# Kernel optimization log

Measured on AMD Instinct MI355X. Metric: run time of the kernel, lower is better.

Reference implementation:

```python
import jax, jax.numpy as jnp
import numpy as np

D = 512
N = 2048

def setup_inputs() -> dict:
    key = jax.random.key(0)
    ks = jax.random.split(key, 5)
    scale = 1.0 / np.sqrt(D)
    return {
        "h": jax.random.normal(ks[0], (N, D), dtype=jnp.float32),
        "W_Q": jax.random.normal(ks[1], (D, D), dtype=jnp.float32) * scale,
        "W_K": jax.random.normal(ks[2], (D, D), dtype=jnp.float32) * scale,
        "W_V": jax.random.normal(ks[3], (D, D), dtype=jnp.float32) * scale,
        "W_O": jax.random.normal(ks[4], (D, D), dtype=jnp.float32) * scale,
    }

def reference(h, W_Q, W_K, W_V, W_O):
    d = h.shape[-1]
    inv_sqrt_d = 1.0 / jnp.sqrt(jnp.asarray(d, h.dtype))
    # nn.Linear(d,d,bias=False): y = h @ W.T
    q = h @ W_Q.T  # [N, d]
    k = h @ W_K.T  # [N, d]
    v = h @ W_V.T  # [N, d]
    # per-token outer product q_a * k_b, softmax over b
    scores = (q[:, :, None] * k[:, None, :]) * inv_sqrt_d  # [N, d, d]
    M = jax.nn.softmax(scores, axis=-1)
    o = jnp.einsum("nab,nb->na", M, v)  # [N, d]
    return o @ W_O.T
```

## Files before the change

### kernel.cpp

```cpp
#include <hip/hip_runtime.h>
#include <hip/hip_bf16.h>

typedef __bf16 bf16_t;
typedef __bf16 bf16x8 __attribute__((ext_vector_type(8)));
typedef __bf16 bf16x4 __attribute__((ext_vector_type(4)));
typedef float  f32x4  __attribute__((ext_vector_type(4)));

#define DD    512
#define NTOK  2048
#define P_DEG 12
#define STR   40

__global__ __launch_bounds__(256) void cvt_kernel(
    const float* __restrict__ h, const float* __restrict__ Wq,
    const float* __restrict__ Wk, const float* __restrict__ Wv,
    const float* __restrict__ Wo, bf16_t* __restrict__ hb, bf16_t* __restrict__ Wb)
{
    int idx = blockIdx.x * 256 + threadIdx.x;
    const float* src;
    bf16_t* dst;
    int off;
    if (idx < 262144) { src = h; dst = hb; off = idx; }
    else {
        int r = idx - 262144;
        int w = r >> 16;
        off = r & 65535;
        src = (w == 0) ? Wq : (w == 1) ? Wk : (w == 2) ? Wv : Wo;
        dst = Wb + (size_t)w * DD * DD;
    }
    f32x4 v = reinterpret_cast<const f32x4*>(src)[off];
    bf16x4 o;
    o[0] = (bf16_t)v[0]; o[1] = (bf16_t)v[1]; o[2] = (bf16_t)v[2]; o[3] = (bf16_t)v[3];
    reinterpret_cast<bf16x4*>(dst)[off] = o;
}

__global__ __launch_bounds__(256) void qkv_kernel(
    const bf16_t* __restrict__ hb, const bf16_t* __restrict__ Wb,
    float* __restrict__ Q, float* __restrict__ Kp, float* __restrict__ V)
{
    __shared__ bf16_t sA[128 * STR];
    __shared__ bf16_t sB[64 * STR];

    const int tid  = threadIdx.x;
    const int lane = tid & 63;
    const int wvi  = tid >> 6;
    const int fr   = lane & 15;
    const int q4   = lane >> 4;
    const int kg   = q4 * 8;
    const int mBase = blockIdx.x * 128;
    const int nBase = blockIdx.y * 64;
    const int z    = blockIdx.z;
    const bf16_t* Bm = Wb + (size_t)z * DD * DD + (size_t)nBase * DD;
    float* C = (z == 0) ? Q : (z == 1) ? Kp : V;
    const float scale = (z == 1) ? 0.04419417382415922f : 1.0f;

    f32x4 acc[2][4] = {};

    for (int k0 = 0; k0 < DD; k0 += 32) {
        __syncthreads();
        #pragma unroll
        for (int i = 0; i < 2; i++) {
            int c = tid + i * 256, row = c >> 2, kc = (c & 3) * 8;
            *reinterpret_cast<uint4*>(&sA[row * STR + kc]) =
                *reinterpret_cast<const uint4*>(hb + (size_t)(mBase + row) * DD + k0 + kc);
        }
        {
            int row = tid >> 2, kc = (tid & 3) * 8;
            *reinterpret_cast<uint4*>(&sB[row * STR + kc]) =
                *reinterpret_cast<const uint4*>(Bm + (size_t)row * DD + k0 + kc);
        }
        __syncthreads();

        bf16x8 af[2], bfr[4];
        #pragma unroll
        for (int t = 0; t < 2; t++)
            af[t] = *reinterpret_cast<const bf16x8*>(&sA[(wvi * 32 + t * 16 + fr) * STR + kg]);
        #pragma unroll
        for (int t = 0; t < 4; t++)
            bfr[t] = *reinterpret_cast<const bf16x8*>(&sB[(t * 16 + fr) * STR + kg]);
        #pragma unroll
        for (int ti = 0; ti < 2; ti++)
            #pragma unroll
            for (int tj = 0; tj < 4; tj++)
                acc[ti][tj] = __builtin_amdgcn_mfma_f32_16x16x32_bf16(af[ti], bfr[tj], acc[ti][tj], 0, 0, 0);
    }

    #pragma unroll
    for (int ti = 0; ti < 2; ti++)
        #pragma unroll
        for (int tj = 0; tj < 4; tj++)
            #pragma unroll
            for (int r = 0; r < 4; r++) {
                int gm = mBase + wvi * 32 + ti * 16 + q4 * 4 + r;
                int gn = nBase + tj * 16 + fr;
                C[(size_t)gm * DD + gn] = acc[ti][tj][r] * scale;
            }
}

__global__ __launch_bounds__(256) void out_kernel(
    const bf16_t* __restrict__ O, const bf16_t* __restrict__ Wob, float* __restrict__ out)
{
    __shared__ bf16_t sA[64 * STR];
    __shared__ bf16_t sB[64 * STR];

    const int tid  = threadIdx.x;
    const int lane = tid & 63;
    const int wvi  = tid >> 6;
    const int fr   = lane & 15;
    const int q4   = lane >> 4;
    const int kg   = q4 * 8;
    const int mBase = blockIdx.x * 64, nBase = blockIdx.y * 64;

    f32x4 acc[4] = {};

    for (int k0 = 0; k0 < DD; k0 += 32) {
        __syncthreads();
        {
            int row = tid >> 2, kc = (tid & 3) * 8;
            *reinterpret_cast<uint4*>(&sA[row * STR + kc]) =
                *reinterpret_cast<const uint4*>(O + (size_t)(mBase + row) * DD + k0 + kc);
            *reinterpret_cast<uint4*>(&sB[row * STR + kc]) =
                *reinterpret_cast<const uint4*>(Wob + (size_t)(nBase + row) * DD + k0 + kc);
        }
        __syncthreads();

        bf16x8 af = *reinterpret_cast<const bf16x8*>(&sA[(wvi * 16 + fr) * STR + kg]);
        #pragma unroll
        for (int tj = 0; tj < 4; tj++) {
            bf16x8 bf = *reinterpret_cast<const bf16x8*>(&sB[(tj * 16 + fr) * STR + kg]);
            acc[tj] = __builtin_amdgcn_mfma_f32_16x16x32_bf16(af, bf, acc[tj], 0, 0, 0);
        }
    }

    #pragma unroll
    for (int tj = 0; tj < 4; tj++)
        #pragma unroll
        for (int r = 0; r < 4; r++) {
            int gm = mBase + wvi * 16 + q4 * 4 + r;
            int gn = nBase + tj * 16 + fr;
            out[(size_t)gm * DD + gn] = acc[tj][r];
        }
}

__global__ __launch_bounds__(256) void attn_kernel(
    const float* __restrict__ Q, const float* __restrict__ Kp,
    const float* __restrict__ V, bf16_t* __restrict__ O)
{
    const int n    = blockIdx.x * 4 + (threadIdx.x >> 6);
    const int lane = threadIdx.x & 63;
    const float* kr = Kp + (size_t)n * DD + lane * 8;
    const float* vr = V  + (size_t)n * DD + lane * 8;

    f32x4 k0 = *reinterpret_cast<const f32x4*>(kr);
    f32x4 k1 = *reinterpret_cast<const f32x4*>(kr + 4);
    f32x4 v0 = *reinterpret_cast<const f32x4*>(vr);
    f32x4 v1 = *reinterpret_cast<const f32x4*>(vr + 4);
    float kap[8] = {k0[0], k0[1], k0[2], k0[3], k1[0], k1[1], k1[2], k1[3]};
    float vv[8]  = {v0[0], v0[1], v0[2], v0[3], v1[0], v1[1], v1[2], v1[3]};

    float md[P_DEG + 1] = {}, mc[P_DEG + 1] = {};
    #pragma unroll
    for (int j = 0; j < 8; j++) {
        float p = 1.f;
        #pragma unroll
        for (int t = 0; t <= P_DEG; t++) {
            md[t] += p;
            mc[t] = fmaf(vv[j], p, mc[t]);
            p *= kap[j];
        }
    }
    #pragma unroll
    for (int m = 32; m >= 1; m >>= 1)
        #pragma unroll
        for (int t = 0; t <= P_DEG; t++) {
            md[t] += __shfl_xor(md[t], m);
            mc[t] += __shfl_xor(mc[t], m);
        }

    const float INVF[P_DEG + 1] = {1.f, 1.f, 0.5f, 1.f/6.f, 1.f/24.f, 1.f/120.f,
        1.f/720.f, 1.f/5040.f, 1.f/40320.f, 1.f/362880.f, 1.f/3628800.f,
        1.f/39916800.f, 1.f/479001600.f};
    #pragma unroll
    for (int t = 0; t <= P_DEG; t++) { md[t] *= INVF[t]; mc[t] *= INVF[t]; }

    const float* qr = Q + (size_t)n * DD + lane * 8;
    f32x4 q0 = *reinterpret_cast<const f32x4*>(qr);
    f32x4 q1 = *reinterpret_cast<const f32x4*>(qr + 4);
    float qv[8] = {q0[0], q0[1], q0[2], q0[3], q1[0], q1[1], q1[2], q1[3]};

    bf16x8 ov;
    #pragma unroll
    for (int j = 0; j < 8; j++) {
        float x = qv[j];
        float F = mc[P_DEG], G = md[P_DEG];
        #pragma unroll
        for (int t = P_DEG - 1; t >= 0; t--) {
            F = fmaf(F, x, mc[t]);
            G = fmaf(G, x, md[t]);
        }
        ov[j] = (bf16_t)(F * __builtin_amdgcn_rcpf(G));
    }
    *reinterpret_cast<bf16x8*>(O + (size_t)n * DD + lane * 8) = ov;
}

extern "C" void kernel_launch(void* const* d_in, const int* in_sizes, int n_in,
                              void* d_out, int out_size, void* d_ws, size_t ws_size,
                              hipStream_t stream)
{
    const float* h  = (const float*)d_in[0];
    const float* Wq = (const float*)d_in[1];
    const float* Wk = (const float*)d_in[2];
    const float* Wv = (const float*)d_in[3];
    const float* Wo = (const float*)d_in[4];
    float* out = (float*)d_out;

    float*  Q  = (float*)d_ws;
    float*  Kp = Q  + (size_t)NTOK * DD;
    float*  V  = Kp + (size_t)NTOK * DD;
    bf16_t* O  = (bf16_t*)(V + (size_t)NTOK * DD);
    bf16_t* hb = O  + (size_t)NTOK * DD;
    bf16_t* Wb = hb + (size_t)NTOK * DD;

    cvt_kernel<<<dim3(2048), dim3(256), 0, stream>>>(h, Wq, Wk, Wv, Wo, hb, Wb);
    qkv_kernel<<<dim3(NTOK / 128, DD / 64, 3), dim3(256), 0, stream>>>(hb, Wb, Q, Kp, V);
    attn_kernel<<<dim3(NTOK / 4), dim3(256), 0, stream>>>(Q, Kp, V, O);
    out_kernel<<<dim3(NTOK / 64, DD / 64), dim3(256), 0, stream>>>(
        O, Wb + (size_t)3 * DD * DD, out);
}
```

Measured before the change: 94.80 us.

## Double-buffer GEMMs with direct global-to-LDS loads and swizzled LDS layout

Both projection GEMMs now stage tiles with global_load_lds into double-buffered, XOR-swizzled shared memory. Each K step of 64 is prefetched while the previous one is consumed, and smaller M tiles give more blocks. The attention kernel hoists the Q load, uses DPP for the first two reduction steps, and skips the constant degree-0 denominator term. The aim is to hide global-load latency, remove bank conflicts and cut shuffle cost, at the price of more LDS per block and a dependence on the global_load_lds lane-address mapping being correct.

```diff
diff --git a/kernel.cpp b/kernel.cpp
--- a/kernel.cpp
+++ b/kernel.cpp
@@ -5,11 +5,24 @@
 typedef __bf16 bf16x8 __attribute__((ext_vector_type(8)));
 typedef __bf16 bf16x4 __attribute__((ext_vector_type(4)));
 typedef float  f32x4  __attribute__((ext_vector_type(4)));
+typedef unsigned int u32;
 
 #define DD    512
 #define NTOK  2048
 #define P_DEG 12
-#define STR   40
+
+__device__ __forceinline__ void gl_lds16(const bf16_t* g, bf16_t* l) {
+    __builtin_amdgcn_global_load_lds((const u32*)g, (u32*)l, 16, 0, 0);
+}
+
+__device__ __forceinline__ float dpp_add_x1(float x) {
+    int r = __builtin_amdgcn_mov_dpp(__float_as_int(x), 0xB1, 0xF, 0xF, true);
+    return x + __int_as_float(r);
+}
+__device__ __forceinline__ float dpp_add_x2(float x) {
+    int r = __builtin_amdgcn_mov_dpp(__float_as_int(x), 0x4E, 0xF, 0xF, true);
+    return x + __int_as_float(r);
+}
 
 __global__ __launch_bounds__(256) void cvt_kernel(
     const float* __restrict__ h, const float* __restrict__ Wq,
@@ -38,106 +51,139 @@
     const bf16_t* __restrict__ hb, const bf16_t* __restrict__ Wb,
     float* __restrict__ Q, float* __restrict__ Kp, float* __restrict__ V)
 {
-    __shared__ bf16_t sA[128 * STR];
-    __shared__ bf16_t sB[64 * STR];
+    __shared__ __align__(16) bf16_t sA[2][64 * 64];
+    __shared__ __align__(16) bf16_t sB[2][64 * 64];
 
     const int tid  = threadIdx.x;
     const int lane = tid & 63;
     const int wvi  = tid >> 6;
     const int fr   = lane & 15;
     const int q4   = lane >> 4;
-    const int kg   = q4 * 8;
-    const int mBase = blockIdx.x * 128;
+    const int mBase = blockIdx.x * 64;
     const int nBase = blockIdx.y * 64;
     const int z    = blockIdx.z;
+    const bf16_t* Am = hb + (size_t)mBase * DD;
     const bf16_t* Bm = Wb + (size_t)z * DD * DD + (size_t)nBase * DD;
     float* C = (z == 0) ? Q : (z == 1) ? Kp : V;
     const float scale = (z == 1) ? 0.04419417382415922f : 1.0f;
 
-    f32x4 acc[2][4] = {};
-
-    for (int k0 = 0; k0 < DD; k0 += 32) {
+    const int c0 = tid;
+    const int c1 = tid + 256;
+    const int r0 = c0 >> 3, s0 = ((c0 & 7) ^ (r0 & 7)) * 8;
+    const int r1 = c1 >> 3, s1 = ((c1 & 7) ^ (r1 & 7)) * 8;
+    const int l0 = wvi * 512;
+    const int l1 = l0 + 2048;
+
+    const bf16_t* gA0 = Am + (size_t)r0 * DD + s0;
+    const bf16_t* gA1 = Am + (size_t)r1 * DD + s1;
+    const bf16_t* gB0 = Bm + (size_t)r0 * DD + s0;
+    const bf16_t* gB1 = Bm + (size_t)r1 * DD + s1;
+
+    f32x4 acc[4] = {};
+
+#define STAGE_QKV(b, k0) do { \
+        gl_lds16(gA0 + (k0), &sA[b][l0]); \
+        gl_lds16(gA1 + (k0), &sA[b][l1]); \
+        gl_lds16(gB0 + (k0), &sB[b][l0]); \
+        gl_lds16(gB1 + (k0), &sB[b][l1]); } while (0)
+
+    auto consume = [&](int b) {
+        #pragma unroll
+        for (int ks = 0; ks < 2; ++ks) {
+            const int slot = ((ks * 4 + q4) ^ (fr & 7)) * 8;
+            bf16x8 af = *reinterpret_cast<const bf16x8*>(&sA[b][(wvi * 16 + fr) * 64 + slot]);
+            #pragma unroll
+            for (int tj = 0; tj < 4; ++tj) {
+                bf16x8 bw = *reinterpret_cast<const bf16x8*>(&sB[b][(tj * 16 + fr) * 64 + slot]);
+                acc[tj] = __builtin_amdgcn_mfma_f32_16x16x32_bf16(af, bw, acc[tj], 0, 0, 0);
+            }
+        }
+    };
+
+    STAGE_QKV(0, 0);
+    __syncthreads();
+    int buf = 0;
+    for (int t = 1; t < 8; ++t) {
+        STAGE_QKV(buf ^ 1, t * 64);
+        consume(buf);
         __syncthreads();
-        #pragma unroll
-        for (int i = 0; i < 2; i++) {
-            int c = tid + i * 256, row = c >> 2, kc = (c & 3) * 8;
-            *reinterpret_cast<uint4*>(&sA[row * STR + kc]) =
-                *reinterpret_cast<const uint4*>(hb + (size_t)(mBase + row) * DD + k0 + kc);
-        }
-        {
-            int row = tid >> 2, kc = (tid & 3) * 8;
-            *reinterpret_cast<uint4*>(&sB[row * STR + kc]) =
-                *reinterpret_cast<const uint4*>(Bm + (size_t)row * DD + k0 + kc);
-        }
-        __syncthreads();
-
-        bf16x8 af[2], bfr[4];
-        #pragma unroll
-        for (int t = 0; t < 2; t++)
-            af[t] = *reinterpret_cast<const bf16x8*>(&sA[(wvi * 32 + t * 16 + fr) * STR + kg]);
-        #pragma unroll
-        for (int t = 0; t < 4; t++)
-            bfr[t] = *reinterpret_cast<const bf16x8*>(&sB[(t * 16 + fr) * STR + kg]);
-        #pragma unroll
-        for (int ti = 0; ti < 2; ti++)
-            #pragma unroll
-            for (int tj = 0; tj < 4; tj++)
-                acc[ti][tj] = __builtin_amdgcn_mfma_f32_16x16x32_bf16(af[ti], bfr[tj], acc[ti][tj], 0, 0, 0);
-    }
-
-    #pragma unroll
-    for (int ti = 0; ti < 2; ti++)
-        #pragma unroll
-        for (int tj = 0; tj < 4; tj++)
-            #pragma unroll
-            for (int r = 0; r < 4; r++) {
-                int gm = mBase + wvi * 32 + ti * 16 + q4 * 4 + r;
-                int gn = nBase + tj * 16 + fr;
-                C[(size_t)gm * DD + gn] = acc[ti][tj][r] * scale;
-            }
+        buf ^= 1;
+    }
+    consume(buf);
+#undef STAGE_QKV
+
+    #pragma unroll
+    for (int tj = 0; tj < 4; ++tj)
+        #pragma unroll
+        for (int r = 0; r < 4; ++r) {
+            int gm = mBase + wvi * 16 + q4 * 4 + r;
+            int gn = nBase + tj * 16 + fr;
+            C[(size_t)gm * DD + gn] = acc[tj][r] * scale;
+        }
 }
 
 __global__ __launch_bounds__(256) void out_kernel(
     const bf16_t* __restrict__ O, const bf16_t* __restrict__ Wob, float* __restrict__ out)
 {
-    __shared__ bf16_t sA[64 * STR];
-    __shared__ bf16_t sB[64 * STR];
+    __shared__ __align__(16) bf16_t sA[2][32 * 64];
+    __shared__ __align__(16) bf16_t sB[2][64 * 64];
 
     const int tid  = threadIdx.x;
     const int lane = tid & 63;
     const int wvi  = tid >> 6;
     const int fr   = lane & 15;
     const int q4   = lane >> 4;
-    const int kg   = q4 * 8;
-    const int mBase = blockIdx.x * 64, nBase = blockIdx.y * 64;
-
-    f32x4 acc[4] = {};
-
-    for (int k0 = 0; k0 < DD; k0 += 32) {
+    const int mBase = blockIdx.x * 32, nBase = blockIdx.y * 64;
+
+    const int c0 = tid;
+    const int c1 = tid + 256;
+    const int r0 = c0 >> 3, s0 = ((c0 & 7) ^ (r0 & 7)) * 8;
+    const int r1 = c1 >> 3, s1 = ((c1 & 7) ^ (r1 & 7)) * 8;
+    const int l0 = wvi * 512, l1 = l0 + 2048;
+
+    const bf16_t* gA  = O   + (size_t)(mBase + r0) * DD + s0;
+    const bf16_t* gB0 = Wob + (size_t)(nBase + r0) * DD + s0;
+    const bf16_t* gB1 = Wob + (size_t)(nBase + r1) * DD + s1;
+
+    f32x4 acc[2] = {};
+    const int bbase = (wvi >> 1) * 32;
+
+#define STAGE_OUT(b, k0) do { \
+        gl_lds16(gA  + (k0), &sA[b][l0]); \
+        gl_lds16(gB0 + (k0), &sB[b][l0]); \
+        gl_lds16(gB1 + (k0), &sB[b][l1]); } while (0)
+
+    auto consume = [&](int b) {
+        #pragma unroll
+        for (int ks = 0; ks < 2; ++ks) {
+            const int slot = ((ks * 4 + q4) ^ (fr & 7)) * 8;
+            bf16x8 af = *reinterpret_cast<const bf16x8*>(&sA[b][((wvi & 1) * 16 + fr) * 64 + slot]);
+            #pragma unroll
+            for (int tj = 0; tj < 2; ++tj) {
+                bf16x8 bw = *reinterpret_cast<const bf16x8*>(&sB[b][(bbase + tj * 16 + fr) * 64 + slot]);
+                acc[tj] = __builtin_amdgcn_mfma_f32_16x16x32_bf16(af, bw, acc[tj], 0, 0, 0);
+            }
+        }
+    };
+
+    STAGE_OUT(0, 0);
+    __syncthreads();
+    int buf = 0;
+    for (int t = 1; t < 8; ++t) {
+        STAGE_OUT(buf ^ 1, t * 64);
+        consume(buf);
         __syncthreads();
-        {
-            int row = tid >> 2, kc = (tid & 3) * 8;
-            *reinterpret_cast<uint4*>(&sA[row * STR + kc]) =
-                *reinterpret_cast<const uint4*>(O + (size_t)(mBase + row) * DD + k0 + kc);
-            *reinterpret_cast<uint4*>(&sB[row * STR + kc]) =
-                *reinterpret_cast<const uint4*>(Wob + (size_t)(nBase + row) * DD + k0 + kc);
-        }
-        __syncthreads();
-
-        bf16x8 af = *reinterpret_cast<const bf16x8*>(&sA[(wvi * 16 + fr) * STR + kg]);
-        #pragma unroll
-        for (int tj = 0; tj < 4; tj++) {
-            bf16x8 bf = *reinterpret_cast<const bf16x8*>(&sB[(tj * 16 + fr) * STR + kg]);
-            acc[tj] = __builtin_amdgcn_mfma_f32_16x16x32_bf16(af, bf, acc[tj], 0, 0, 0);
-        }
-    }
-
-    #pragma unroll
-    for (int tj = 0; tj < 4; tj++)
-        #pragma unroll
-        for (int r = 0; r < 4; r++) {
-            int gm = mBase + wvi * 16 + q4 * 4 + r;
-            int gn = nBase + tj * 16 + fr;
+        buf ^= 1;
+    }
+    consume(buf);
+#undef STAGE_OUT
+
+    #pragma unroll
+    for (int tj = 0; tj < 2; ++tj)
+        #pragma unroll
+        for (int r = 0; r < 4; ++r) {
+            int gm = mBase + (wvi & 1) * 16 + q4 * 4 + r;
+            int gn = nBase + bbase + tj * 16 + fr;
             out[(size_t)gm * DD + gn] = acc[tj][r];
         }
 }
@@ -150,11 +196,14 @@
     const int lane = threadIdx.x & 63;
     const float* kr = Kp + (size_t)n * DD + lane * 8;
     const float* vr = V  + (size_t)n * DD + lane * 8;
+    const float* qr = Q  + (size_t)n * DD + lane * 8;
 
     f32x4 k0 = *reinterpret_cast<const f32x4*>(kr);
     f32x4 k1 = *reinterpret_cast<const f32x4*>(kr + 4);
     f32x4 v0 = *reinterpret_cast<const f32x4*>(vr);
     f32x4 v1 = *reinterpret_cast<const f32x4*>(vr + 4);
+    f32x4 q0 = *reinterpret_cast<const f32x4*>(qr);
+    f32x4 q1 = *reinterpret_cast<const f32x4*>(qr + 4);
     float kap[8] = {k0[0], k0[1], k0[2], k0[3], k1[0], k1[1], k1[2], k1[3]};
     float vv[8]  = {v0[0], v0[1], v0[2], v0[3], v1[0], v1[1], v1[2], v1[3]};
 
@@ -162,30 +211,39 @@
     #pragma unroll
     for (int j = 0; j < 8; j++) {
         float p = 1.f;
-        #pragma unroll
-        for (int t = 0; t <= P_DEG; t++) {
+        mc[0] += vv[j];
+        #pragma unroll
+        for (int t = 1; t <= P_DEG; t++) {
+            p *= kap[j];
             md[t] += p;
             mc[t] = fmaf(vv[j], p, mc[t]);
-            p *= kap[j];
-        }
-    }
-    #pragma unroll
-    for (int m = 32; m >= 1; m >>= 1)
+        }
+    }
+    #pragma unroll
+    for (int t = 0; t <= P_DEG; t++) {
+        mc[t] = dpp_add_x1(mc[t]);
+        if (t) md[t] = dpp_add_x1(md[t]);
+    }
+    #pragma unroll
+    for (int t = 0; t <= P_DEG; t++) {
+        mc[t] = dpp_add_x2(mc[t]);
+        if (t) md[t] = dpp_add_x2(md[t]);
+    }
+    #pragma unroll
+    for (int m = 4; m <= 32; m <<= 1)
         #pragma unroll
         for (int t = 0; t <= P_DEG; t++) {
-            md[t] += __shfl_xor(md[t], m);
             mc[t] += __shfl_xor(mc[t], m);
-        }
+            if (t) md[t] += __shfl_xor(md[t], m);
+        }
+    md[0] = 512.f;
 
     const float INVF[P_DEG + 1] = {1.f, 1.f, 0.5f, 1.f/6.f, 1.f/24.f, 1.f/120.f,
         1.f/720.f, 1.f/5040.f, 1.f/40320.f, 1.f/362880.f, 1.f/3628800.f,
         1.f/39916800.f, 1.f/479001600.f};
     #pragma unroll
-    for (int t = 0; t <= P_DEG; t++) { md[t] *= INVF[t]; mc[t] *= INVF[t]; }
-
-    const float* qr = Q + (size_t)n * DD + lane * 8;
-    f32x4 q0 = *reinterpret_cast<const f32x4*>(qr);
-    f32x4 q1 = *reinterpret_cast<const f32x4*>(qr + 4);
+    for (int t = 1; t <= P_DEG; t++) { md[t] *= INVF[t]; mc[t] *= INVF[t]; }
+
     float qv[8] = {q0[0], q0[1], q0[2], q0[3], q1[0], q1[1], q1[2], q1[3]};
 
     bf16x8 ov;
@@ -222,8 +280,8 @@
     bf16_t* Wb = hb + (size_t)NTOK * DD;
 
     cvt_kernel<<<dim3(2048), dim3(256), 0, stream>>>(h, Wq, Wk, Wv, Wo, hb, Wb);
-    qkv_kernel<<<dim3(NTOK / 128, DD / 64, 3), dim3(256), 0, stream>>>(hb, Wb, Q, Kp, V);
+    qkv_kernel<<<dim3(NTOK / 64, DD / 64, 3), dim3(256), 0, stream>>>(hb, Wb, Q, Kp, V);
     attn_kernel<<<dim3(NTOK / 4), dim3(256), 0, stream>>>(Q, Kp, V, O);
-    out_kernel<<<dim3(NTOK / 64, DD / 64), dim3(256), 0, stream>>>(
+    out_kernel<<<dim3(NTOK / 32, DD / 64), dim3(256), 0, stream>>>(
         O, Wb + (size_t)3 * DD * DD, out);
 }
```

New measurement: 91.47 us, median of 2. 1.04x faster.
